# Optimization experiments

Hardware: AMD Instinct MI355X
Metric: run time of the kernel (lower is better)

The kernel has to match this reference:

```python
import jax, jax.numpy as jnp
import numpy as np

# ---- config (matches init_kwargs) ----
B, N = 2, 192
NCG, L0, L1, ANUM = 16, 16, 8, 2
RAD_MAXR, NB, H = 4.0, 10, 32
SQ2 = 1.4142135623730951

RS0 = {0: NCG}
RS_HID = {0: L0, 1: L1}
RS_FIN = {0: ANUM, 1: ANUM}
LMAX_SH = 2


def relu_r(x):  # rescaled_act.relu: unit second moment under N(0,1)
    return jax.nn.relu(x) * SQ2


def sigmoid_r(x):  # rescaled_act.sigmoid
    return jax.nn.sigmoid(x) * 1.84623


def _cg():
    # Real-basis coupling tensors C[i_out, j_in, m_filter]; l=1 components ordered (y,z,x).
    c000 = np.ones((1, 1, 1))
    eye3 = np.eye(3)
    c101 = (eye3 / np.sqrt(3.0)).reshape(3, 1, 3)
    c011 = (eye3 / np.sqrt(3.0)).reshape(1, 3, 3)
    c110 = (eye3 / np.sqrt(3.0)).reshape(3, 3, 1)
    eps = np.zeros((3, 3, 3))
    for i, j, k in [(0, 1, 2), (1, 2, 0), (2, 0, 1)]:
        eps[i, j, k] = 1.0
        eps[j, i, k] = -1.0
    c111 = eps / np.sqrt(6.0)
    c = 1.0925484305920792
    b = 0.31539156525252005
    d = 0.5462742152960396
    m = np.zeros((3, 3, 5))  # index 0=y, 1=z, 2=x
    m[2, 0, 0] = m[0, 2, 0] = c / 2            # ~ x*y
    m[0, 1, 1] = m[1, 0, 1] = c / 2            # ~ y*z
    m[1, 1, 2] = 2 * b; m[0, 0, 2] = -b; m[2, 2, 2] = -b  # ~ 2z^2-x^2-y^2
    m[2, 1, 3] = m[1, 2, 3] = c / 2            # ~ x*z
    m[2, 2, 4] = d; m[0, 0, 4] = -d            # ~ x^2-y^2
    c112 = m / np.linalg.norm(m)
    return {(0, 0, 0): c000, (1, 0, 1): c101, (0, 1, 1): c011,
            (1, 1, 0): c110, (1, 1, 1): c111, (1, 1, 2): c112}

CG = {k: jnp.asarray(v, jnp.float32) for k, v in _cg().items()}


def paths_for(rs_in, rs_out):
    out = []
    for lo in sorted(rs_out):
        for li in sorted(rs_in):
            for lf in range(abs(lo - li), min(lo + li, LMAX_SH) + 1):
                out.append((lo, li, lf, rs_out[lo], rs_in[li]))
    return out


def total_w(rs_in, rs_out):
    return sum(mo * mi for _, _, _, mo, mi in paths_for(rs_in, rs_out))


def convolution(feat, geo, w0, b0, wout, rs_in, rs_out):
    # feat: dict l -> [B,N,mul,2l+1]; geo: [B,N,3]
    rel = geo[:, :, None, :] - geo[:, None, :, :]              # [B,N,N,3]
    r = jnp.sqrt(jnp.sum(rel * rel, -1) + 1e-12)               # [B,N,N]
    u = rel / jnp.maximum(r, 1e-6)[..., None]
    x_, y_, z_ = u[..., 0], u[..., 1], u[..., 2]
    Y = {0: jnp.full(r.shape + (1,), 0.28209479177387814, r.dtype),
         1: 0.4886025119029199 * jnp.stack([y_, z_, x_], -1),
         2: jnp.stack([1.0925484305920792 * x_ * y_,
                       1.0925484305920792 * y_ * z_,
                       0.31539156525252005 * (2 * z_ * z_ - x_ * x_ - y_ * y_),
                       1.0925484305920792 * x_ * z_,
                       0.5462742152960396 * (x_ * x_ - y_ * y_)], -1)}
    # CosineBasisModel: overlapping cos^2 bumps on [0, RAD_MAXR]
    centers = jnp.linspace(0.0, RAD_MAXR, NB)
    step = RAD_MAXR / (NB - 1)
    dg = (r[..., None] - centers) / step
    basis = jnp.where(jnp.abs(dg) < 1.0, jnp.cos(0.5 * jnp.pi * dg) ** 2, 0.0)
    h = relu_r(basis @ (w0 / np.sqrt(NB)) + b0)                # [B,N,N,H]
    Rw = h @ (wout / np.sqrt(H))                               # [B,N,N,total_w]

    plist = paths_for(rs_in, rs_out)
    npaths = {lo: sum(1 for p in plist if p[0] == lo) for lo in rs_out}
    out = {lo: jnp.zeros(geo.shape[:2] + (rs_out[lo], 2 * lo + 1), geo.dtype)
           for lo in rs_out}
    off = 0
    for lo, li, lf, mo, mi in plist:
        w = Rw[..., off:off + mo * mi].reshape(Rw.shape[:3] + (mo, mi))
        off += mo * mi
        contrib = jnp.einsum('zabuv,zabm,ijm,zbvj->zaui', w, Y[lf],
                             CG[(lo, li, lf)], feat[li], optimize=True)
        out[lo] = out[lo] + contrib / np.sqrt(mi * npaths[lo])
    return out


def gated_block(feat, geo, w0, b0, wout, rs_in, rs_out):
    n_gates = sum(m for l, m in rs_out.items() if l > 0)
    rs_conv = dict(rs_out)
    rs_conv[0] = rs_out.get(0, 0) + n_gates
    c = convolution(feat, geo, w0, b0, wout, rs_in, rs_conv)
    m0 = rs_out.get(0, 0)
    out = {0: relu_r(c[0][:, :, :m0])}
    gates = sigmoid_r(c[0][:, :, m0:])                         # [B,N,n_gates,1]
    g_off = 0
    for l in sorted(rs_out):
        if l == 0:
            continue
        ml = rs_out[l]
        out[l] = c[l] * gates[:, :, g_off:g_off + ml]
        g_off += ml
    return out


def _forward(features, geometry, c0_w0, c0_b0, c0_wout, c1_w0, c1_b0, c1_wout,
             c2_w0, c2_b0, c2_wout):
    s = 1.0 / np.sqrt(N)  # output.div(geometry.size(1)**0.5) before every layer
    f = {0: features[..., None] * s}
    f = gated_block(f, geometry, c0_w0, c0_b0, c0_wout, RS0, RS_HID)
    f = {l: v * s for l, v in f.items()}
    f = gated_block(f, geometry, c1_w0, c1_b0, c1_wout, RS_HID, RS_HID)
    f = {l: v * s for l, v in f.items()}
    f = convolution(f, geometry, c2_w0, c2_b0, c2_wout, RS_HID, RS_FIN)
    # final Rs = [(1,0),(1,1)] * atomic_nums -> interleave scalar+vector per species
    out = jnp.concatenate([f[0], f[1]], axis=-1)               # [B,N,ANUM,4]
    return out.reshape(B, N, ANUM * 4)


def setup_inputs() -> dict:
    key = jax.random.key(0)
    ks = jax.random.split(key, 8)
    RS_G = {0: L0 + L1, 1: L1}  # gated conv output: scalars + gates, then l=1
    return {
        'features': jax.random.normal(ks[0], (B, N, NCG), jnp.float32),
        'geometry': jax.random.normal(ks[1], (B, N, 3), jnp.float32),
        'c0_w0': jax.random.normal(ks[2], (NB, H), jnp.float32),
        'c0_b0': jnp.zeros((H,), jnp.float32),
        'c0_wout': jax.random.normal(ks[3], (H, total_w(RS0, RS_G)), jnp.float32),
        'c1_w0': jax.random.normal(ks[4], (NB, H), jnp.float32),
        'c1_b0': jnp.zeros((H,), jnp.float32),
        'c1_wout': jax.random.normal(ks[5], (H, total_w(RS_HID, RS_G)), jnp.float32),
        'c2_w0': jax.random.normal(ks[6], (NB, H), jnp.float32),
        'c2_b0': jnp.zeros((H,), jnp.float32),
        'c2_wout': jax.random.normal(ks[7], (H, total_w(RS_HID, RS_FIN)), jnp.float32),
    }


def reference(features, geometry, c0_w0, c0_b0, c0_wout, c1_w0, c1_b0, c1_wout,
              c2_w0, c2_b0, c2_wout):
    return _forward(features, geometry, c0_w0, c0_b0, c0_wout,
                    c1_w0, c1_b0, c1_wout, c2_w0, c2_b0, c2_wout)
```

## Files before the change

kernel.cpp:

```cpp
#include <hip/hip_runtime.h>
#include <math.h>


#define NN 192
#define BB 2
#define SPLIT 8
#define NS 24
#define NBASIS 10
#define HHID 32

__device__ __forceinline__ float relu_r(float x) {
    return fmaxf(x, 0.0f) * 1.4142135623730951f;
}
__device__ __forceinline__ float sigmoid_r(float x) {
    return (1.0f / (1.0f + expf(-x))) * 1.84623f;
}

#define S_SCALE 0.07216878364870323f
#define ISQ10   0.31622776601683794f
#define I32     0.1767766952966369f

template <int LAYER>
__global__ __launch_bounds__(256, 4) void tfn_s1(
    const float* __restrict__ fin,
    const float* __restrict__ geo,
    const float* __restrict__ w0g,
    const float* __restrict__ b0g,
    const float* __restrict__ wout,
    float* __restrict__ part)
{
    constexpr int TC    = (LAYER == 0) ? 64 : 144;
    constexpr int TSTR  = (LAYER == 0) ? 64 : 160;
    constexpr int TW    = (LAYER == 0) ? 512 : (LAYER == 1 ? 896 : 128);
    constexpr int NOUT  = (LAYER == 2) ? 8 : 48;
    constexpr int MSTRE = (LAYER == 0) ? 68 : 148;
    constexpr int R     = (LAYER == 0) ? 2 : 4;
    constexpr int C     = (LAYER == 0) ? 4 : 5;

    constexpr int oT   = 0;
    constexpr int oF0  = oT + NS * TSTR;
    constexpr int oF1  = oF0 + NS * 16;
    constexpr int oY   = oF1 + ((LAYER == 0) ? 0 : NS * 24);
    constexpr int oBas = oY + NS * 8;
    constexpr int oH   = oBas + NS * NBASIS;
    constexpr int SM0  = oH + NS * HHID;
    constexpr int oU   = 32 * MSTRE;
    constexpr int SMe  = oU + NOUT * 33;
    constexpr int SM   = (SM0 > SMe) ? SM0 : SMe;
    __shared__ float sm[SM];

    const int tid  = threadIdx.x;
    const int blk  = blockIdx.x;
    const int sp   = blk & (SPLIT - 1);
    const int atom = blk >> 3;
    const int z    = atom / NN, a = atom % NN;
    const int nb0  = sp * NS;

    if constexpr (LAYER == 0) {
        for (int i = tid; i < NS * 16; i += 256)
            sm[oF0 + i] = fin[(z * NN + nb0) * 16 + i] * S_SCALE;
    } else {
        for (int idx4 = tid; idx4 < NS * 12; idx4 += 256) {
            int loc = idx4 / 12, q = idx4 - loc * 12;
            const float4* p = (const float4*)&fin[((z * NN + nb0 + loc) * SPLIT) * 48 + q * 4];
            float4 s4;
            float4 v0 = p[0],  v1 = p[12], v2 = p[24], v3 = p[36];
            float4 v4 = p[48], v5 = p[60], v6 = p[72], v7 = p[84];
            s4.x = ((v0.x + v1.x) + (v2.x + v3.x)) + ((v4.x + v5.x) + (v6.x + v7.x));
            s4.y = ((v0.y + v1.y) + (v2.y + v3.y)) + ((v4.y + v5.y) + (v6.y + v7.y));
            s4.z = ((v0.z + v1.z) + (v2.z + v3.z)) + ((v4.z + v5.z) + (v6.z + v7.z));
            s4.w = ((v0.w + v1.w) + (v2.w + v3.w)) + ((v4.w + v5.w) + (v6.w + v7.w));
            *(float4*)&sm[oT + loc * 48 + q * 4] = s4;
        }
    }
    {
        const float ax = geo[(z * NN + a) * 3 + 0];
        const float ay = geo[(z * NN + a) * 3 + 1];
        const float az = geo[(z * NN + a) * 3 + 2];
        for (int idx = tid; idx < NS * 12; idx += 256) {
            int bl = idx / 12, it = idx - bl * 12;
            const float* gb = &geo[(z * NN + nb0 + bl) * 3];
            float rx = ax - gb[0], ry = ay - gb[1], rz = az - gb[2];
            float r = sqrtf(rx * rx + ry * ry + rz * rz + 1e-12f);
            if (it < NBASIS) {
                float dg = r * 2.25f - (float)it;
                float bas = 0.0f;
                if (fabsf(dg) < 1.0f) {
                    float cc = cosf(1.5707963267948966f * dg);
                    bas = cc * cc;
                }
                sm[oBas + bl * NBASIS + it] = bas;
            } else {
                float inv = 1.0f / fmaxf(r, 1e-6f);
                float ux = rx * inv, uy = ry * inv, uz = rz * inv;
                if (it == 10) {
                    sm[oY + bl * 8 + 0] = 0.4886025119029199f * uy;
                    sm[oY + bl * 8 + 1] = 0.4886025119029199f * uz;
                    sm[oY + bl * 8 + 2] = 0.4886025119029199f * ux;
                } else {
                    sm[oY + bl * 8 + 3] = 1.0925484305920792f * ux * uy;
                    sm[oY + bl * 8 + 4] = 1.0925484305920792f * uy * uz;
                    sm[oY + bl * 8 + 5] = 0.31539156525252005f * (2.0f * uz * uz - ux * ux - uy * uy);
                    sm[oY + bl * 8 + 6] = 1.0925484305920792f * ux * uz;
                    sm[oY + bl * 8 + 7] = 0.5462742152960396f * (ux * ux - uy * uy);
                }
            }
        }
    }
    __syncthreads();

#pragma unroll
    for (int rp = 0; rp < 3; ++rp) {
        int idx = rp * 256 + tid;
        int bl = idx >> 5, j = idx & 31;
        float su = 0.0f;
#pragma unroll
        for (int k = 0; k < NBASIS; ++k)
            su += sm[oBas + bl * NBASIS + k] * w0g[k * HHID + j];
        sm[oH + idx] = relu_r(su * ISQ10 + b0g[j]);
    }
    if constexpr (LAYER != 0) {
        for (int idx = tid; idx < NS * 40; idx += 256) {
            int loc = idx / 40, c2 = idx - loc * 40;
            const float* cs = &sm[oT + loc * 48];
            if (c2 < 16) {
                sm[oF0 + loc * 16 + c2] = relu_r(cs[c2]) * S_SCALE;
            } else {
                int j = c2 - 16;
                sm[oF1 + loc * 24 + j] = cs[24 + j] * sigmoid_r(cs[16 + (j & 7)]) * S_SCALE;
            }
        }
    }
    __syncthreads();

    if constexpr (LAYER == 0) {
        for (int idx = tid; idx < NS * 16; idx += 256) {
            int loc = idx >> 4, c = idx & 15;
            sm[oT + loc * TSTR + c] = 0.28209479177387814f * sm[oF0 + loc * 16 + c];
        }
#pragma unroll
        for (int i2 = 0; i2 < 3; ++i2)
            for (int idx = tid; idx < NS * 16; idx += 256) {
                int loc = idx >> 4, v = idx & 15;
                sm[oT + loc * TSTR + 16 + i2 * 16 + v] =
                    sm[oY + loc * 8 + i2] * sm[oF0 + loc * 16 + v] * 0.5773502691896258f;
            }
    } else {
        for (int idx = tid; idx < NS * 16; idx += 256) {
            int loc = idx >> 4, c = idx & 15;
            sm[oT + loc * TSTR + c] = 0.28209479177387814f * sm[oF0 + loc * 16 + c];
        }
        for (int idx = tid; idx < NS * 8; idx += 256) {
            int loc = idx >> 3, u = idx & 7;
            const float* Yb = &sm[oY + loc * 8];
            const float* fT = &sm[oF1 + loc * 24];
            sm[oT + loc * TSTR + 16 + u] =
                (fT[u] * Yb[0] + fT[8 + u] * Yb[1] + fT[16 + u] * Yb[2]) * 0.5773502691896258f;
        }
#pragma unroll
        for (int i2 = 0; i2 < 3; ++i2)
            for (int idx = tid; idx < NS * 16; idx += 256) {
                int loc = idx >> 4, v = idx & 15;
                sm[oT + loc * TSTR + 24 + i2 * 16 + v] =
                    sm[oY + loc * 8 + i2] * sm[oF0 + loc * 16 + v] * 0.5773502691896258f;
            }
        for (int idx = tid; idx < NS * 24; idx += 256) {
            int loc = idx / 24, j = idx - loc * 24;
            sm[oT + loc * TSTR + 72 + j] =
                sm[oF1 + loc * 24 + j] * (0.28209479177387814f * 0.5773502691896258f);
        }
#pragma unroll
        for (int i2 = 0; i2 < 3; ++i2) {
            const int i1 = (i2 + 1) % 3, i3 = (i2 + 2) % 3;
            for (int idx = tid; idx < NS * 8; idx += 256) {
                int loc = idx >> 3, u = idx & 7;
                const float* Yb = &sm[oY + loc * 8];
                const float* fT = &sm[oF1 + loc * 24];
                sm[oT + loc * TSTR + 96 + i2 * 8 + u] =
                    (fT[i1 * 8 + u] * Yb[i3] - fT[i3 * 8 + u] * Yb[i1]) * 0.4082482904638631f;
            }
        }
#pragma unroll
        for (int i2 = 0; i2 < 3; ++i2)
            for (int idx = tid; idx < NS * 8; idx += 256) {
                int loc = idx >> 3, u = idx & 7;
                const float* Yb = &sm[oY + loc * 8];
                const float* fT = &sm[oF1 + loc * 24];
                const float D  = 0.31622776601683794f;
                const float Bc = 0.18257418583505536f;
                float f0v = fT[u], f1v = fT[8 + u], f2v = fT[16 + u];
                float Y20 = Yb[3], Y21 = Yb[4], Y22 = Yb[5], Y23 = Yb[6], Y24 = Yb[7];
                float val;
                if (i2 == 0)      val = D * (Y20 * f2v + Y21 * f1v) - (Bc * Y22 + D * Y24) * f0v;
                else if (i2 == 1) val = D * (Y21 * f0v + Y23 * f2v) + 2.0f * Bc * Y22 * f1v;
                else              val = D * (Y20 * f0v + Y23 * f1v + Y24 * f2v) - Bc * Y22 * f2v;
                sm[oT + loc * TSTR + 120 + i2 * 8 + u] = val;
            }
    }
    __syncthreads();

    float acc[R][C];
#pragma unroll
    for (int rr = 0; rr < R; ++rr)
#pragma unroll
        for (int cc = 0; cc < C; ++cc) acc[rr][cc] = 0.0f;

    if constexpr (LAYER == 0) {
        const int hr = tid >> 4, cg = tid & 15;
#pragma unroll 4
        for (int bl = 0; bl < NS; ++bl) {
            float2 hv = *(const float2*)&sm[oH + bl * 32 + hr * 2];
            float4 tv = *(const float4*)&sm[oT + bl * 64 + cg * 4];
            float hvv[2] = {hv.x, hv.y};
            float tvv[4] = {tv.x, tv.y, tv.z, tv.w};
#pragma unroll
            for (int rr = 0; rr < 2; ++rr)
#pragma unroll
                for (int cc = 0; cc < 4; ++cc) acc[rr][cc] += hvv[rr] * tvv[cc];
        }
    } else {
        const int hr = tid >> 5, cg = tid & 31;
#pragma unroll 4
        for (int bl = 0; bl < NS; ++bl) {
            float4 hv = *(const float4*)&sm[oH + bl * 32 + hr * 4];
            const float* tp = &sm[oT + bl * TSTR + cg * 5];
            float hvv[4] = {hv.x, hv.y, hv.z, hv.w};
            float t0 = tp[0], t1 = tp[1], t2 = tp[2], t3 = tp[3], t4 = tp[4];
#pragma unroll
            for (int rr = 0; rr < 4; ++rr) {
                acc[rr][0] += hvv[rr] * t0;
                acc[rr][1] += hvv[rr] * t1;
                acc[rr][2] += hvv[rr] * t2;
                acc[rr][3] += hvv[rr] * t3;
                acc[rr][4] += hvv[rr] * t4;
            }
        }
    }
    __syncthreads();

    {
        const int hr = (LAYER == 0) ? (tid >> 4) : (tid >> 5);
        const int cg = (LAYER == 0) ? (tid & 15) : (tid & 31);
#pragma unroll
        for (int rr = 0; rr < R; ++rr)
#pragma unroll
            for (int cc = 0; cc < C; ++cc) {
                int col = cg * C + cc;
                if (col < TC) sm[(hr * R + rr) * MSTRE + col] = acc[rr][cc];
            }
    }
    __syncthreads();

    constexpr int NITEM = NOUT * 32;
    for (int rp = 0; rp < NITEM / 256; ++rp) {
        int idx = rp * 256 + tid;
        int h = idx / NOUT, o = idx - h * NOUT;
        const float* wr = &wout[h * TW];
        const float* mr = &sm[h * MSTRE];
        float U;
        if constexpr (LAYER == 0) {
            const float sc = I32 * 0.25f;
            float accv = 0.0f;
            if (o < 24) {
#pragma unroll
                for (int v = 0; v < 16; ++v) accv += wr[o * 16 + v] * mr[v];
            } else {
                int j = o - 24, u = j & 7, i2 = j >> 3;
#pragma unroll
                for (int v = 0; v < 16; ++v) accv += wr[384 + u * 16 + v] * mr[16 + i2 * 16 + v];
            }
            U = accv * sc;
        } else if constexpr (LAYER == 1) {
            float aA = 0.0f, aB = 0.0f;
            if (o < 24) {
#pragma unroll
                for (int v = 0; v < 16; ++v) aA += wr[o * 16 + v] * mr[v];
#pragma unroll
                for (int v = 0; v < 8; ++v) aB += wr[384 + o * 8 + v] * mr[16 + v];
                U = (aA * I32 + aB * 0.25f) * I32;
            } else {
                int j = o - 24, u = j & 7, i2 = j >> 3;
#pragma unroll
                for (int v = 0; v < 16; ++v) aA += wr[576 + u * 16 + v] * mr[24 + i2 * 16 + v];
#pragma unroll
                for (int v = 0; v < 8; ++v)
                    aB += wr[704 + u * 8 + v] * mr[72 + i2 * 8 + v]
                        + wr[768 + u * 8 + v] * mr[96 + i2 * 8 + v]
                        + wr[832 + u * 8 + v] * mr[120 + i2 * 8 + v];
                U = (aA * 0.125f + aB * I32) * I32;
            }
        } else {
            float aA = 0.0f, aB = 0.0f;
            if (o < 2) {
#pragma unroll
                for (int v = 0; v < 16; ++v) aA += wr[o * 16 + v] * mr[v];
#pragma unroll
                for (int v = 0; v < 8; ++v) aB += wr[32 + o * 8 + v] * mr[16 + v];
                U = (aA * I32 + aB * 0.25f) * I32;
            } else {
                int j = o - 2, u = j & 1, i2 = j >> 1;
#pragma unroll
                for (int v = 0; v < 16; ++v) aA += wr[48 + u * 16 + v] * mr[24 + i2 * 16 + v];
#pragma unroll
                for (int v = 0; v < 8; ++v)
                    aB += wr[80 + u * 8 + v] * mr[72 + i2 * 8 + v]
                        + wr[96 + u * 8 + v] * mr[96 + i2 * 8 + v]
                        + wr[112 + u * 8 + v] * mr[120 + i2 * 8 + v];
                U = (aA * 0.125f + aB * I32) * I32;
            }
        }
        sm[oU + o * 33 + h] = U;
    }
    __syncthreads();

    if (tid < NOUT) {
        float su = 0.0f;
#pragma unroll
        for (int h = 0; h < 32; ++h) su += sm[oU + tid * 33 + h];
        part[blk * NOUT + tid] = su;
    }
}

__global__ __launch_bounds__(256) void tfn_fin(
    const float* __restrict__ part2, float* __restrict__ out)
{
    int t = blockIdx.x * 256 + threadIdx.x;
    int atom = t >> 3, o = t & 7;
    const float* p = &part2[atom * SPLIT * 8];
    float su = ((p[o] + p[8 + o]) + (p[16 + o] + p[24 + o]))
             + ((p[32 + o] + p[40 + o]) + (p[48 + o] + p[56 + o]));
    int pos;
    if (o < 2) pos = o * 4;
    else { int j = o - 2; int i2 = j >> 1, u = j & 1; pos = u * 4 + 1 + i2; }
    out[atom * 8 + pos] = su;
}

template <int LAYER>
__global__ __launch_bounds__(256) void tfn_layer_mono(
    const float* __restrict__ geo,
    const float* __restrict__ fin0,
    const float* __restrict__ fin1,
    const float* __restrict__ w0,
    const float* __restrict__ b0g,
    const float* __restrict__ wout,
    float* __restrict__ o0,
    float* __restrict__ o1)
{
    constexpr int TC   = (LAYER == 0) ? 64 : 144;
    constexpr int TW   = (LAYER == 0) ? 512 : (LAYER == 1 ? 896 : 128);
    constexpr int CPT  = TC / 8;
    constexpr int CPTT = TC / 16;

    const int tid = threadIdx.x;
    const int blk = blockIdx.x;
    const int z = blk / NN, a = blk % NN;

    __shared__ float geoL[NN * 3];
    __shared__ float f0L[NN * 16];
    __shared__ float f1L[(LAYER == 0) ? 1 : (NN * 24)];
    __shared__ float w0L[NBASIS * HHID];
    __shared__ float b0L[HHID];
    __shared__ float YC[16 * 8];
    __shared__ float basC[16 * NBASIS];
    __shared__ float hC[16 * HHID];
    __shared__ float tC[16 * TC];
    __shared__ float Mlds[HHID * TC];
    __shared__ float outS[32];

    const float s = S_SCALE;

    for (int i = tid; i < NN * 3; i += 256) geoL[i] = geo[z * NN * 3 + i];
    for (int i = tid; i < NN * 16; i += 256) {
        float v = fin0[z * NN * 16 + i];
        if (LAYER == 0) v *= s;
        f0L[i] = v;
    }
    if constexpr (LAYER != 0) {
        for (int i = tid; i < NN * 24; i += 256) f1L[i] = fin1[z * NN * 24 + i];
    }
    for (int i = tid; i < NBASIS * HHID; i += 256) w0L[i] = w0[i];
    if (tid < HHID) b0L[tid] = b0g[tid];
    __syncthreads();

    const float ax = geoL[a * 3 + 0], ay = geoL[a * 3 + 1], az = geoL[a * 3 + 2];

    float Macc[CPT];
#pragma unroll
    for (int j = 0; j < CPT; ++j) Macc[j] = 0.0f;
    const int hh  = tid >> 3;
    const int cg0 = (tid & 7) * CPT;

    for (int cb = 0; cb < NN / 16; ++cb) {
        {
            const int bl = tid & 15, item = tid >> 4;
            const int b = cb * 16 + bl;
            float rx = ax - geoL[b * 3 + 0];
            float ry = ay - geoL[b * 3 + 1];
            float rz = az - geoL[b * 3 + 2];
            float r = sqrtf(rx * rx + ry * ry + rz * rz + 1e-12f);
            float inv = 1.0f / fmaxf(r, 1e-6f);
            float ux = rx * inv, uy = ry * inv, uz = rz * inv;
            if (item < NBASIS) {
                float dg = r * 2.25f - (float)item;
                float bas = 0.0f;
                if (fabsf(dg) < 1.0f) {
                    float cc = cosf(1.5707963267948966f * dg);
                    bas = cc * cc;
                }
                basC[bl * NBASIS + item] = bas;
            } else if (item == 10) {
                YC[bl * 8 + 0] = 0.4886025119029199f * uy;
                YC[bl * 8 + 1] = 0.4886025119029199f * uz;
                YC[bl * 8 + 2] = 0.4886025119029199f * ux;
            } else if (item == 11) {
                YC[bl * 8 + 3] = 1.0925484305920792f * ux * uy;
                YC[bl * 8 + 4] = 1.0925484305920792f * uy * uz;
                YC[bl * 8 + 5] = 0.31539156525252005f * (2.0f * uz * uz - ux * ux - uy * uy);
                YC[bl * 8 + 6] = 1.0925484305920792f * ux * uz;
                YC[bl * 8 + 7] = 0.5462742152960396f * (ux * ux - uy * uy);
            }
        }
        __syncthreads();

#pragma unroll
        for (int rep = 0; rep < 2; ++rep) {
            int idx = tid + rep * 256;
            int bl = idx >> 5, h2 = idx & 31;
            float su = 0.0f;
#pragma unroll
            for (int k = 0; k < NBASIS; ++k) su += basC[bl * NBASIS + k] * w0L[k * HHID + h2];
            hC[bl * HHID + h2] = relu_r(su * ISQ10 + b0L[h2]);
        }

        {
            const int bl = tid >> 4, cg = tid & 15;
            const int b = cb * 16 + bl;
            const float* Yb = &YC[bl * 8];
#pragma unroll
            for (int jj = 0; jj < CPTT; ++jj) {
                int c = cg * CPTT + jj;
                float val;
                if constexpr (LAYER == 0) {
                    if (c < 16) {
                        val = 0.28209479177387814f * f0L[b * 16 + c];
                    } else {
                        int q = c - 16, v = q / 3, i2 = q % 3;
                        val = Yb[i2] * f0L[b * 16 + v] * 0.5773502691896258f;
                    }
                } else {
                    if (c < 16) {
                        val = 0.28209479177387814f * f0L[b * 16 + c];
                    } else if (c < 24) {
                        int v = c - 16;
                        const float* f = &f1L[(b * 8 + v) * 3];
                        val = (f[0] * Yb[0] + f[1] * Yb[1] + f[2] * Yb[2]) * 0.5773502691896258f;
                    } else if (c < 72) {
                        int q = c - 24, v = q / 3, i2 = q % 3;
                        val = Yb[i2] * f0L[b * 16 + v] * 0.5773502691896258f;
                    } else if (c < 96) {
                        int q = c - 72, v = q / 3, i2 = q % 3;
                        val = f1L[(b * 8 + v) * 3 + i2] * (0.28209479177387814f * 0.5773502691896258f);
                    } else if (c < 120) {
                        int q = c - 96, v = q / 3, i2 = q % 3;
                        const float* f = &f1L[(b * 8 + v) * 3];
                        int i1 = (i2 + 1) % 3, i3 = (i2 + 2) % 3;
                        val = (f[i1] * Yb[i3] - f[i3] * Yb[i1]) * 0.4082482904638631f;
                    } else {
                        int q = c - 120, v = q / 3, i2 = q % 3;
                        const float* f = &f1L[(b * 8 + v) * 3];
                        const float D = 0.31622776601683794f;
                        const float Bc = 0.18257418583505536f;
                        float Y20 = Yb[3], Y21 = Yb[4], Y22 = Yb[5], Y23 = Yb[6], Y24 = Yb[7];
                        if (i2 == 0)      val = D * (Y20 * f[2] + Y21 * f[1]) - (Bc * Y22 + D * Y24) * f[0];
                        else if (i2 == 1) val = D * (Y21 * f[0] + Y23 * f[2]) + 2.0f * Bc * Y22 * f[1];
                        else              val = D * (Y20 * f[0] + Y23 * f[1] + Y24 * f[2]) - Bc * Y22 * f[2];
                    }
                }
                tC[bl * TC + c] = val;
            }
        }
        __syncthreads();

#pragma unroll 4
        for (int bl = 0; bl < 16; ++bl) {
            float hv = hC[bl * HHID + hh];
#pragma unroll
            for (int j = 0; j < CPT; ++j) Macc[j] += hv * tC[bl * TC + cg0 + j];
        }
        __syncthreads();
    }

#pragma unroll
    for (int j = 0; j < CPT; ++j) Mlds[hh * TC + cg0 + j] = Macc[j];
    __syncthreads();

    const float i32 = I32;

    if constexpr (LAYER == 0) {
        const float sc = i32 * 0.25f;
        float o1v = 0.0f;
        if (tid < 24) {
            float acc = 0.0f;
            for (int h2 = 0; h2 < 32; ++h2) {
                const float* wr = &wout[h2 * TW + tid * 16];
                const float* mr = &Mlds[h2 * TC];
#pragma unroll
                for (int v = 0; v < 16; ++v) acc += wr[v] * mr[v];
            }
            outS[tid] = acc * sc;
        } else if (tid >= 32 && tid < 56) {
            int idx = tid - 32, u = idx / 3, i2 = idx % 3;
            float acc = 0.0f;
            for (int h2 = 0; h2 < 32; ++h2) {
                const float* wr = &wout[h2 * TW + 384 + u * 16];
                const float* mr = &Mlds[h2 * TC + 16 + i2];
#pragma unroll
                for (int v = 0; v < 16; ++v) acc += wr[v] * mr[v * 3];
            }
            o1v = acc * sc;
        }
        __syncthreads();
        if (tid < 16) {
            o0[(z * NN + a) * 16 + tid] = relu_r(outS[tid]) * s;
        } else if (tid >= 32 && tid < 56) {
            int idx = tid - 32, u = idx / 3, i2 = idx % 3;
            float g = sigmoid_r(outS[16 + u]);
            o1[((z * NN + a) * 8 + u) * 3 + i2] = o1v * g * s;
        }
    } else if constexpr (LAYER == 1) {
        float o1v = 0.0f;
        if (tid < 24) {
            float aA = 0.0f, aB = 0.0f;
            for (int h2 = 0; h2 < 32; ++h2) {
                const float* wr = &wout[h2 * TW];
                const float* mr = &Mlds[h2 * TC];
#pragma unroll
                for (int v = 0; v < 16; ++v) aA += wr[tid * 16 + v] * mr[v];
#pragma unroll
                for (int v = 0; v < 8; ++v) aB += wr[384 + tid * 8 + v] * mr[16 + v];
            }
            outS[tid] = (aA * i32 + aB * 0.25f) * i32;
        } else if (tid >= 32 && tid < 56) {
            int idx = tid - 32, u = idx / 3, i2 = idx % 3;
            float aA = 0.0f, aB = 0.0f;
            for (int h2 = 0; h2 < 32; ++h2) {
                const float* wr = &wout[h2 * TW];
                const float* mr = &Mlds[h2 * TC];
#pragma unroll
                for (int v = 0; v < 16; ++v) aA += wr[576 + u * 16 + v] * mr[24 + v * 3 + i2];
#pragma unroll
                for (int v = 0; v < 8; ++v)
                    aB += wr[704 + u * 8 + v] * mr[72 + v * 3 + i2]
                        + wr[768 + u * 8 + v] * mr[96 + v * 3 + i2]
                        + wr[832 + u * 8 + v] * mr[120 + v * 3 + i2];
            }
            o1v = (aA * 0.125f + aB * i32) * i32;
        }
        __syncthreads();
        if (tid < 16) {
            o0[(z * NN + a) * 16 + tid] = relu_r(outS[tid]) * s;
        } else if (tid >= 32 && tid < 56) {
            int idx = tid - 32, u = idx / 3, i2 = idx % 3;
            float g = sigmoid_r(outS[16 + u]);
            o1[((z * NN + a) * 8 + u) * 3 + i2] = o1v * g * s;
        }
    } else {
        if (tid < 2) {
            float aA = 0.0f, aB = 0.0f;
            for (int h2 = 0; h2 < 32; ++h2) {
                const float* wr = &wout[h2 * TW];
                const float* mr = &Mlds[h2 * TC];
#pragma unroll
                for (int v = 0; v < 16; ++v) aA += wr[tid * 16 + v] * mr[v];
#pragma unroll
                for (int v = 0; v < 8; ++v) aB += wr[32 + tid * 8 + v] * mr[16 + v];
            }
            o0[(z * NN + a) * 8 + tid * 4] = (aA * i32 + aB * 0.25f) * i32;
        } else if (tid >= 32 && tid < 38) {
            int idx = tid - 32, u = idx / 3, i2 = idx % 3;
            float aA = 0.0f, aB = 0.0f;
            for (int h2 = 0; h2 < 32; ++h2) {
                const float* wr = &wout[h2 * TW];
                const float* mr = &Mlds[h2 * TC];
#pragma unroll
                for (int v = 0; v < 16; ++v) aA += wr[48 + u * 16 + v] * mr[24 + v * 3 + i2];
#pragma unroll
                for (int v = 0; v < 8; ++v)
                    aB += wr[80 + u * 8 + v] * mr[72 + v * 3 + i2]
                        + wr[96 + u * 8 + v] * mr[96 + v * 3 + i2]
                        + wr[112 + u * 8 + v] * mr[120 + v * 3 + i2];
            }
            o0[(z * NN + a) * 8 + u * 4 + 1 + i2] = (aA * 0.125f + aB * i32) * i32;
        }
    }
}

extern "C" void kernel_launch(void* const* d_in, const int* in_sizes, int n_in,
                              void* d_out, int out_size, void* d_ws, size_t ws_size,
                              hipStream_t stream) {
    const float* features = (const float*)d_in[0];
    const float* geometry = (const float*)d_in[1];
    const float* c0w0   = (const float*)d_in[2];
    const float* c0b0   = (const float*)d_in[3];
    const float* c0wout = (const float*)d_in[4];
    const float* c1w0   = (const float*)d_in[5];
    const float* c1b0   = (const float*)d_in[6];
    const float* c1wout = (const float*)d_in[7];
    const float* c2w0   = (const float*)d_in[8];
    const float* c2b0   = (const float*)d_in[9];
    const float* c2wout = (const float*)d_in[10];
    float* out = (float*)d_out;

    float* ws = (float*)d_ws;
    const size_t NBLK = (size_t)BB * NN * SPLIT;
    const size_t need = NBLK * 48 * 2 + NBLK * 8;

    if (ws_size >= need * sizeof(float)) {
        float* partA = ws;
        float* partB = partA + NBLK * 48;
        float* part2 = partB + NBLK * 48;

        dim3 g1((unsigned)NBLK), blk(256);
        hipLaunchKernelGGL((tfn_s1<0>), g1, blk, 0, stream,
                           features, geometry, c0w0, c0b0, c0wout, partA);
        hipLaunchKernelGGL((tfn_s1<1>), g1, blk, 0, stream,
                           partA, geometry, c1w0, c1b0, c1wout, partB);
        hipLaunchKernelGGL((tfn_s1<2>), g1, blk, 0, stream,
                           partB, geometry, c2w0, c2b0, c2wout, part2);
        hipLaunchKernelGGL(tfn_fin, dim3(BB * NN * 8 / 256), blk, 0, stream,
                           part2, out);
    } else {
        float* f0a = ws;
        float* f1a = f0a + BB * NN * 16;
        float* f0b = f1a + BB * NN * 24;
        float* f1b = f0b + BB * NN * 16;
        dim3 grid(BB * NN), blk(256);
        hipLaunchKernelGGL((tfn_layer_mono<0>), grid, blk, 0, stream,
                           geometry, features, nullptr, c0w0, c0b0, c0wout, f0a, f1a);
        hipLaunchKernelGGL((tfn_layer_mono<1>), grid, blk, 0, stream,
                           geometry, f0a, f1a, c1w0, c1b0, c1wout, f0b, f1b);
        hipLaunchKernelGGL((tfn_layer_mono<2>), grid, blk, 0, stream,
                           geometry, f0b, f1b, c2w0, c2b0, c2wout, out, nullptr);
    }
}
```

Measured before the change: 121.8 us.

## Move split-reduction and gated activation into a separate per-atom kernel

Adds a small tfn_act kernel that sums the SPLIT partial outputs per atom and applies the relu and sigmoid gate once, writing compact activated features. Layers 1 and 2 then load those precomputed features instead of each block re-reducing eight partials for its 24 neighbours and recomputing the activations, which removes redundant global reads and transcendental work. The TSTR padding also changes from 160 to 168, likely to reduce shared-memory bank conflicts. The cost is two extra kernel launches and an extra global round trip between layers.

```diff
diff --git a/kernel.cpp b/kernel.cpp
--- a/kernel.cpp
+++ b/kernel.cpp
@@ -20,9 +20,34 @@
 #define ISQ10   0.31622776601683794f
 #define I32     0.1767766952966369f
 
+__global__ __launch_bounds__(256) void tfn_act(
+    const float* __restrict__ part, float* __restrict__ fa0, float* __restrict__ fa1)
+{
+    int t = blockIdx.x * 256 + threadIdx.x;
+    if (t >= BB * NN * 40) return;
+    int atom = t / 40, c = t - atom * 40;
+    const float* p = &part[atom * SPLIT * 48];
+    if (c < 16) {
+        float s = 0.0f;
+#pragma unroll
+        for (int sp = 0; sp < SPLIT; ++sp) s += p[sp * 48 + c];
+        fa0[atom * 16 + c] = relu_r(s) * S_SCALE;
+    } else {
+        int j = c - 16, u = j & 7;
+        float g = 0.0f, v = 0.0f;
+#pragma unroll
+        for (int sp = 0; sp < SPLIT; ++sp) {
+            g += p[sp * 48 + 16 + u];
+            v += p[sp * 48 + 24 + j];
+        }
+        fa1[atom * 24 + j] = v * sigmoid_r(g) * S_SCALE;
+    }
+}
+
 template <int LAYER>
 __global__ __launch_bounds__(256, 4) void tfn_s1(
-    const float* __restrict__ fin,
+    const float* __restrict__ fin0,
+    const float* __restrict__ fin1,
     const float* __restrict__ geo,
     const float* __restrict__ w0g,
     const float* __restrict__ b0g,
@@ -30,7 +55,7 @@
     float* __restrict__ part)
 {
     constexpr int TC    = (LAYER == 0) ? 64 : 144;
-    constexpr int TSTR  = (LAYER == 0) ? 64 : 160;
+    constexpr int TSTR  = (LAYER == 0) ? 64 : 168;
     constexpr int TW    = (LAYER == 0) ? 512 : (LAYER == 1 ? 896 : 128);
     constexpr int NOUT  = (LAYER == 2) ? 8 : 48;
     constexpr int MSTRE = (LAYER == 0) ? 68 : 148;
@@ -58,20 +83,12 @@
 
     if constexpr (LAYER == 0) {
         for (int i = tid; i < NS * 16; i += 256)
-            sm[oF0 + i] = fin[(z * NN + nb0) * 16 + i] * S_SCALE;
+            sm[oF0 + i] = fin0[(z * NN + nb0) * 16 + i] * S_SCALE;
     } else {
-        for (int idx4 = tid; idx4 < NS * 12; idx4 += 256) {
-            int loc = idx4 / 12, q = idx4 - loc * 12;
-            const float4* p = (const float4*)&fin[((z * NN + nb0 + loc) * SPLIT) * 48 + q * 4];
-            float4 s4;
-            float4 v0 = p[0],  v1 = p[12], v2 = p[24], v3 = p[36];
-            float4 v4 = p[48], v5 = p[60], v6 = p[72], v7 = p[84];
-            s4.x = ((v0.x + v1.x) + (v2.x + v3.x)) + ((v4.x + v5.x) + (v6.x + v7.x));
-            s4.y = ((v0.y + v1.y) + (v2.y + v3.y)) + ((v4.y + v5.y) + (v6.y + v7.y));
-            s4.z = ((v0.z + v1.z) + (v2.z + v3.z)) + ((v4.z + v5.z) + (v6.z + v7.z));
-            s4.w = ((v0.w + v1.w) + (v2.w + v3.w)) + ((v4.w + v5.w) + (v6.w + v7.w));
-            *(float4*)&sm[oT + loc * 48 + q * 4] = s4;
-        }
+        for (int i = tid; i < NS * 16; i += 256)
+            sm[oF0 + i] = fin0[(z * NN + nb0) * 16 + i];
+        for (int i = tid; i < NS * 24; i += 256)
+            sm[oF1 + i] = fin1[(z * NN + nb0) * 24 + i];
     }
     {
         const float ax = geo[(z * NN + a) * 3 + 0];
@@ -118,18 +135,6 @@
         for (int k = 0; k < NBASIS; ++k)
             su += sm[oBas + bl * NBASIS + k] * w0g[k * HHID + j];
         sm[oH + idx] = relu_r(su * ISQ10 + b0g[j]);
-    }
-    if constexpr (LAYER != 0) {
-        for (int idx = tid; idx < NS * 40; idx += 256) {
-            int loc = idx / 40, c2 = idx - loc * 40;
-            const float* cs = &sm[oT + loc * 48];
-            if (c2 < 16) {
-                sm[oF0 + loc * 16 + c2] = relu_r(cs[c2]) * S_SCALE;
-            } else {
-                int j = c2 - 16;
-                sm[oF1 + loc * 24 + j] = cs[24 + j] * sigmoid_r(cs[16 + (j & 7)]) * S_SCALE;
-            }
-        }
     }
     __syncthreads();
 
@@ -612,21 +617,29 @@
     float* out = (float*)d_out;
 
     float* ws = (float*)d_ws;
-    const size_t NBLK = (size_t)BB * NN * SPLIT;
-    const size_t need = NBLK * 48 * 2 + NBLK * 8;
+    const size_t NBLK  = (size_t)BB * NN * SPLIT;
+    const size_t NATOM = (size_t)BB * NN;
+    const size_t need  = NBLK * 48 * 2 + NBLK * 8 + NATOM * 40 * 2;
 
     if (ws_size >= need * sizeof(float)) {
         float* partA = ws;
         float* partB = partA + NBLK * 48;
         float* part2 = partB + NBLK * 48;
+        float* fa0A  = part2 + NBLK * 8;
+        float* fa1A  = fa0A + NATOM * 16;
+        float* fa0B  = fa1A + NATOM * 24;
+        float* fa1B  = fa0B + NATOM * 16;
 
         dim3 g1((unsigned)NBLK), blk(256);
+        dim3 gact((unsigned)((NATOM * 40 + 255) / 256));
         hipLaunchKernelGGL((tfn_s1<0>), g1, blk, 0, stream,
-                           features, geometry, c0w0, c0b0, c0wout, partA);
+                           features, nullptr, geometry, c0w0, c0b0, c0wout, partA);
+        hipLaunchKernelGGL(tfn_act, gact, blk, 0, stream, partA, fa0A, fa1A);
         hipLaunchKernelGGL((tfn_s1<1>), g1, blk, 0, stream,
-                           partA, geometry, c1w0, c1b0, c1wout, partB);
+                           fa0A, fa1A, geometry, c1w0, c1b0, c1wout, partB);
+        hipLaunchKernelGGL(tfn_act, gact, blk, 0, stream, partB, fa0B, fa1B);
         hipLaunchKernelGGL((tfn_s1<2>), g1, blk, 0, stream,
-                           partB, geometry, c2w0, c2b0, c2wout, part2);
+                           fa0B, fa1B, geometry, c2w0, c2b0, c2wout, part2);
         hipLaunchKernelGGL(tfn_fin, dim3(BB * NN * 8 / 256), blk, 0, stream,
                            part2, out);
     } else {
```

Result: no change. 120.4 us (-1.1%).
